# Performance work log

Measured on AMD Instinct MI355X. Metric: run time of the kernel, lower is better.

The kernel has to match this reference:

```python
import jax, jax.numpy as jnp
import numpy as np

B, C = 8192, 4096

def _to_complex(r):
    # (..., 2) real/imag stack -> complex
    return jax.lax.complex(r[..., 0], r[..., 1])

def _to_real(z):
    return jnp.stack([jnp.real(z), jnp.imag(z)], axis=-1)

def setup_inputs() -> dict:
    key = jax.random.key(0)
    kx, ka, kd = jax.random.split(key, 3)
    x = jax.random.normal(kx, (B, C, 2), dtype=jnp.float32)
    # A, D ~ Normal(1.0, 0.01) per reset_parameters
    A = 1.0 + 0.01 * jax.random.normal(ka, (1, C, 2), dtype=jnp.float32)
    D = 1.0 + 0.01 * jax.random.normal(kd, (1, C, 2), dtype=jnp.float32)
    return {"x": x, "A": A, "D": D}

def reference(x, A, D):
    # Elementwise scale (real and imag parts scaled independently, NOT complex mul)
    xs = A * x                                   # (B, C, 2)
    # torch.fft(x, 1): complex FFT over the signal dim (channels, dim 1)
    f = jnp.fft.fft(_to_complex(xs), axis=1)     # (B, C) complex64
    fs = D * _to_real(f)                         # elementwise scale in real/imag repr
    # torch.ifft is normalized by 1/N, same as jnp.fft.ifft
    out = jnp.fft.ifft(_to_complex(fs), axis=1)  # (B, C) complex64
    return _to_real(out)                         # (B, C, 2)
```

## Files before the change

### kernel.cpp

```cpp
#include <hip/hip_runtime.h>
#include <hip/hip_bf16.h>

#define FFT_N   4096
#define THREADS 256

__device__ __forceinline__ float2 cmul(float2 a, float2 b) {
    return make_float2(a.x*b.x - a.y*b.y, a.x*b.y + a.y*b.x);
}
__device__ __forceinline__ float2 cadd(float2 a, float2 b){ return make_float2(a.x+b.x, a.y+b.y); }
__device__ __forceinline__ float2 csub(float2 a, float2 b){ return make_float2(a.x-b.x, a.y-b.y); }

template<int S>
__device__ __forceinline__ float2 muli(float2 z) {
    return (S < 0) ? make_float2(z.y, -z.x) : make_float2(-z.y, z.x);
}

template<int S>
__device__ __forceinline__ void dft4(float2 a0, float2 a1, float2 a2, float2 a3,
                                     float2& y0, float2& y1, float2& y2, float2& y3) {
    float2 e0 = cadd(a0, a2), e1 = cadd(a1, a3);
    float2 o0 = csub(a0, a2), o1 = muli<S>(csub(a1, a3));
    y0 = cadd(e0, e1); y2 = csub(e0, e1);
    y1 = cadd(o0, o1); y3 = csub(o0, o1);
}

template<int S>
__device__ __forceinline__ void dft16(float2* a) {
    const float C1 = 0.92387953251128674f;
    const float S1 = 0.38268343236508978f;
    const float R2 = 0.70710678118654752f;
    const float sg = (S < 0) ? -1.0f : 1.0f;
    const float2 w1 = make_float2( C1,  sg*S1);
    const float2 w2 = make_float2( R2,  sg*R2);
    const float2 w3 = make_float2( S1,  sg*C1);
    const float2 w6 = make_float2(-R2,  sg*R2);
    const float2 w9 = make_float2(-C1, -sg*S1);
    float2 t[16];
    dft4<S>(a[0], a[4], a[8],  a[12], t[0],  t[1],  t[2],  t[3]);
    dft4<S>(a[1], a[5], a[9],  a[13], t[4],  t[5],  t[6],  t[7]);
    dft4<S>(a[2], a[6], a[10], a[14], t[8],  t[9],  t[10], t[11]);
    dft4<S>(a[3], a[7], a[11], a[15], t[12], t[13], t[14], t[15]);
    t[5]  = cmul(t[5],  w1);  t[6]  = cmul(t[6],  w2);  t[7]  = cmul(t[7],  w3);
    t[9]  = cmul(t[9],  w2);  t[10] = muli<S>(t[10]);   t[11] = cmul(t[11], w6);
    t[13] = cmul(t[13], w3);  t[14] = cmul(t[14], w6);  t[15] = cmul(t[15], w9);
    dft4<S>(t[0], t[4], t[8],  t[12], a[0], a[4], a[8],  a[12]);
    dft4<S>(t[1], t[5], t[9],  t[13], a[1], a[5], a[9],  a[13]);
    dft4<S>(t[2], t[6], t[10], t[14], a[2], a[6], a[10], a[14]);
    dft4<S>(t[3], t[7], t[11], t[15], a[3], a[7], a[11], a[15]);
}

template<int S>
__device__ __forceinline__ void twiddle_apply(float2* R, int p, float invM) {
    float ang = ((S < 0) ? -6.283185307179586f : 6.283185307179586f) * (float)p * invM;
    float s, c;
    __sincosf(ang, &s, &c);
    float2 w1 = make_float2(c, s);
    float2 w = w1;
    R[1] = cmul(R[1], w);
    #pragma unroll
    for (int k = 2; k < 16; ++k) { w = cmul(w, w1); R[k] = cmul(R[k], w); }
}

__device__ __forceinline__ int pidx(int i) { return i + (i >> 4); }

__global__ __launch_bounds__(THREADS, 4) void afdf_fft_kernel(
    const float* __restrict__ x,
    const float* __restrict__ A,
    const float* __restrict__ D,
    float* __restrict__ out)
{
    __shared__ float2 sh[4352];

    const int t = threadIdx.x;
    const size_t rb = (size_t)blockIdx.x * FFT_N;
    const float2* __restrict__ xr = (const float2*)x + rb;
    const float2* __restrict__ Ac = (const float2*)A;
    const float2* __restrict__ Dc = (const float2*)D;
    float2* __restrict__ o        = (float2*)out + rb;

    float2 r[16];

    {
        const int p = t;
        #pragma unroll
        for (int n1 = 0; n1 < 16; ++n1) {
            float2 v = xr[p + 256*n1];
            float2 a = Ac[p + 256*n1];
            r[n1] = make_float2(a.x*v.x, a.y*v.y);
        }
        dft16<-1>(r);
        twiddle_apply<-1>(r, p, 1.0f/4096.0f);
        #pragma unroll
        for (int k = 0; k < 16; ++k) sh[pidx(p + 256*k)] = r[k];
    }
    __syncthreads();

    {
        const int b = t >> 4, p2 = t & 15, base = b*256;
        #pragma unroll
        for (int n1 = 0; n1 < 16; ++n1) r[n1] = sh[pidx(base + p2 + 16*n1)];
        dft16<-1>(r);
        twiddle_apply<-1>(r, p2, 1.0f/256.0f);
        #pragma unroll
        for (int k = 0; k < 16; ++k) sh[pidx(base + p2 + 16*k)] = r[k];
    }
    __syncthreads();

    {
        const int base = 16*t;
        #pragma unroll
        for (int n = 0; n < 16; ++n) r[n] = sh[pidx(base + n)];
        dft16<-1>(r);
        const int k1 = t >> 4, k2 = t & 15;
        #pragma unroll
        for (int k3 = 0; k3 < 16; ++k3) {
            float2 d = Dc[256*k3 + 16*k2 + k1];
            r[k3] = make_float2(d.x*r[k3].x, d.y*r[k3].y);
        }
        dft16<+1>(r);
        #pragma unroll
        for (int n = 0; n < 16; ++n) sh[pidx(base + n)] = r[n];
    }
    __syncthreads();

    {
        const int b = t >> 4, p2 = t & 15, base = b*256;
        #pragma unroll
        for (int k = 0; k < 16; ++k) r[k] = sh[pidx(base + p2 + 16*k)];
        twiddle_apply<+1>(r, p2, 1.0f/256.0f);
        dft16<+1>(r);
        #pragma unroll
        for (int n1 = 0; n1 < 16; ++n1) sh[pidx(base + p2 + 16*n1)] = r[n1];
    }
    __syncthreads();

    {
        const int p = t;
        #pragma unroll
        for (int k = 0; k < 16; ++k) r[k] = sh[pidx(p + 256*k)];
        twiddle_apply<+1>(r, p, 1.0f/4096.0f);
        dft16<+1>(r);
        const float inv = 1.0f / 4096.0f;
        #pragma unroll
        for (int n1 = 0; n1 < 16; ++n1)
            o[p + 256*n1] = make_float2(r[n1].x*inv, r[n1].y*inv);
    }
}

extern "C" void kernel_launch(void* const* d_in, const int* in_sizes, int n_in,
                              void* d_out, int out_size, void* d_ws, size_t ws_size,
                              hipStream_t stream) {
    (void)in_sizes; (void)n_in; (void)out_size; (void)d_ws; (void)ws_size;
    const float* x = (const float*)d_in[0];
    const float* A = (const float*)d_in[1];
    const float* D = (const float*)d_in[2];
    float* out = (float*)d_out;

    afdf_fft_kernel<<<dim3(8192), dim3(THREADS), 0, stream>>>(x, A, D, out);
}
```

Measured before the change: 498.1 us.

## Replace padded LDS layout with XOR swizzle and vectorized float4 LDS access

Replaces the padded shared-memory indexing with an XOR swizzle over an unpadded 4096-entry buffer. This lets the middle stage read and write contiguous 16-element rows as float4 while still avoiding bank conflicts. It also computes twiddle powers in a shorter dependency chain, raises the launch-bounds occupancy hint from 4 to 5 blocks, and drops the unused bf16 header. The smaller LDS footprint and the occupancy hint aim for more resident blocks, at the risk of register pressure or spills from the twiddle array.

```diff
diff --git a/kernel.cpp b/kernel.cpp
--- a/kernel.cpp
+++ b/kernel.cpp
@@ -1,5 +1,4 @@
 #include <hip/hip_runtime.h>
-#include <hip/hip_bf16.h>
 
 #define FFT_N   4096
 #define THREADS 256
@@ -51,25 +50,30 @@
 
 template<int S>
 __device__ __forceinline__ void twiddle_apply(float2* R, int p, float invM) {
-    float ang = ((S < 0) ? -6.283185307179586f : 6.283185307179586f) * (float)p * invM;
+    float ang = 6.283185307179586f * (float)p * invM;
+    if (S < 0) ang = -ang;
     float s, c;
     __sincosf(ang, &s, &c);
-    float2 w1 = make_float2(c, s);
-    float2 w = w1;
-    R[1] = cmul(R[1], w);
+    float2 w[16];
+    w[1] = make_float2(c, s);
+    w[2] = cmul(w[1], w[1]);
+    w[3] = cmul(w[2], w[1]);
+    w[4] = cmul(w[2], w[2]);
     #pragma unroll
-    for (int k = 2; k < 16; ++k) { w = cmul(w, w1); R[k] = cmul(R[k], w); }
+    for (int k = 5; k < 16; ++k) w[k] = cmul(w[k-4], w[4]);
+    #pragma unroll
+    for (int k = 1; k < 16; ++k) R[k] = cmul(R[k], w[k]);
 }
 
-__device__ __forceinline__ int pidx(int i) { return i + (i >> 4); }
+__device__ __forceinline__ int swz(int i) { return i ^ (((i >> 4) & 7) << 1); }
 
-__global__ __launch_bounds__(THREADS, 4) void afdf_fft_kernel(
+__global__ __launch_bounds__(THREADS, 5) void afdf_fft_kernel(
     const float* __restrict__ x,
     const float* __restrict__ A,
     const float* __restrict__ D,
     float* __restrict__ out)
 {
-    __shared__ float2 sh[4352];
+    __shared__ __align__(16) float2 sh[FFT_N];
 
     const int t = threadIdx.x;
     const size_t rb = (size_t)blockIdx.x * FFT_N;
@@ -82,6 +86,7 @@
 
     {
         const int p = t;
+        const int pa = p ^ (((p >> 4) & 7) << 1);
         #pragma unroll
         for (int n1 = 0; n1 < 16; ++n1) {
             float2 v = xr[p + 256*n1];
@@ -91,25 +96,30 @@
         dft16<-1>(r);
         twiddle_apply<-1>(r, p, 1.0f/4096.0f);
         #pragma unroll
-        for (int k = 0; k < 16; ++k) sh[pidx(p + 256*k)] = r[k];
+        for (int k = 0; k < 16; ++k) sh[pa + 256*k] = r[k];
     }
     __syncthreads();
 
     {
         const int b = t >> 4, p2 = t & 15, base = b*256;
         #pragma unroll
-        for (int n1 = 0; n1 < 16; ++n1) r[n1] = sh[pidx(base + p2 + 16*n1)];
+        for (int n1 = 0; n1 < 16; ++n1) r[n1] = sh[swz(base + p2 + 16*n1)];
         dft16<-1>(r);
         twiddle_apply<-1>(r, p2, 1.0f/256.0f);
         #pragma unroll
-        for (int k = 0; k < 16; ++k) sh[pidx(base + p2 + 16*k)] = r[k];
+        for (int k = 0; k < 16; ++k) sh[swz(base + p2 + 16*k)] = r[k];
     }
     __syncthreads();
 
     {
-        const int base = 16*t;
+        const int cb = 16*t;
+        const int u  = (t & 7) << 1;
         #pragma unroll
-        for (int n = 0; n < 16; ++n) r[n] = sh[pidx(base + n)];
+        for (int m = 0; m < 8; ++m) {
+            float4 v = *reinterpret_cast<const float4*>(&sh[cb + ((2*m) ^ u)]);
+            r[2*m]   = make_float2(v.x, v.y);
+            r[2*m+1] = make_float2(v.z, v.w);
+        }
         dft16<-1>(r);
         const int k1 = t >> 4, k2 = t & 15;
         #pragma unroll
@@ -119,25 +129,29 @@
         }
         dft16<+1>(r);
         #pragma unroll
-        for (int n = 0; n < 16; ++n) sh[pidx(base + n)] = r[n];
+        for (int m = 0; m < 8; ++m) {
+            float4 v = make_float4(r[2*m].x, r[2*m].y, r[2*m+1].x, r[2*m+1].y);
+            *reinterpret_cast<float4*>(&sh[cb + ((2*m) ^ u)]) = v;
+        }
     }
     __syncthreads();
 
     {
         const int b = t >> 4, p2 = t & 15, base = b*256;
         #pragma unroll
-        for (int k = 0; k < 16; ++k) r[k] = sh[pidx(base + p2 + 16*k)];
+        for (int k = 0; k < 16; ++k) r[k] = sh[swz(base + p2 + 16*k)];
         twiddle_apply<+1>(r, p2, 1.0f/256.0f);
         dft16<+1>(r);
         #pragma unroll
-        for (int n1 = 0; n1 < 16; ++n1) sh[pidx(base + p2 + 16*n1)] = r[n1];
+        for (int n1 = 0; n1 < 16; ++n1) sh[swz(base + p2 + 16*n1)] = r[n1];
     }
     __syncthreads();
 
     {
         const int p = t;
+        const int pa = p ^ (((p >> 4) & 7) << 1);
         #pragma unroll
-        for (int k = 0; k < 16; ++k) r[k] = sh[pidx(p + 256*k)];
+        for (int k = 0; k < 16; ++k) r[k] = sh[pa + 256*k];
         twiddle_apply<+1>(r, p, 1.0f/4096.0f);
         dft16<+1>(r);
         const float inv = 1.0f / 4096.0f;
```

New measurement: 504.3 us. About the same (+1.2%).
